# Performance work log

Measured on AMD Instinct MI355X. Metric: run time of the kernel, lower is better.

The kernel has to match this reference:

```python
import jax, jax.numpy as jnp
import numpy as np
from jax import lax

B, T = 256, 256
FD = (768, 74, 35)      # text, audio, vision input feature dims
HD = (128, 64, 64)      # LSTM hidden sizes
LEN = sum(HD)           # 256, fused feature dim
TW = 2                  # time_window
EXT = TW * LEN + 1      # 513, extended_dim
RANK = 24
OUT = 1


def setup_inputs() -> dict:
    key = jax.random.key(0)
    ks = iter(jax.random.split(key, 32))
    def n(shape, scale=0.05):
        return jax.random.normal(next(ks), shape, dtype=jnp.float32) * scale
    inp = {
        "text": n((B, T, FD[0]), 1.0),
        "audio": n((B, T, FD[1]), 1.0),
        "vision": n((B, T, FD[2]), 1.0),
    }
    # LSTM params per subnet: W_ih [4H, D], W_hh [4H, H], combined bias [4H]
    for tag, d, h in (("t", FD[0], HD[0]), ("a", FD[1], HD[1]), ("v", FD[2], HD[2])):
        inp[f"Wih_{tag}"] = n((4 * h, d))
        inp[f"Whh_{tag}"] = n((4 * h, h))
        inp[f"b_{tag}"] = n((4 * h,))
    inp["W1"] = n((RANK * OUT, LEN))
    inp["b1"] = n((RANK * OUT,))
    inp["W2"] = n((RANK * OUT, EXT))
    inp["b2"] = n((RANK * OUT,))
    inp["fw"] = n((1, RANK), 1.0)  # fusion_weights, xavier_normal-like
    return inp


def _lstm_seq(x, Wih, Whh, b):
    # x: [B, T, D] -> all hidden states [B, T, H]; torch gate order i,f,g,o
    Bn = x.shape[0]
    H = Whh.shape[1]
    h0 = jnp.zeros((Bn, H), x.dtype)
    def step(carry, xt):
        h, c = carry
        g = xt @ Wih.T + h @ Whh.T + b
        i, f, gg, o = jnp.split(g, 4, axis=-1)
        c = jax.nn.sigmoid(f) * c + jax.nn.sigmoid(i) * jnp.tanh(gg)
        h = jax.nn.sigmoid(o) * jnp.tanh(c)
        return (h, c), h
    _, hs = lax.scan(step, (h0, h0), jnp.swapaxes(x, 0, 1))
    return jnp.swapaxes(hs, 0, 1)


def reference(text, audio, vision,
              Wih_t, Whh_t, b_t, Wih_a, Whh_a, b_a, Wih_v, Whh_v, b_v,
              W1, b1, W2, b2, fw):
    # SubNets (dropout is identity in eval mode)
    audio_h = _lstm_seq(audio, Wih_a, Whh_a, b_a)
    video_h = _lstm_seq(vision, Wih_v, Whh_v, b_v)
    text_h = _lstm_seq(text, Wih_t, Whh_t, b_t)
    z = jnp.concatenate((audio_h, video_h, text_h), axis=2)  # [B, T, LEN]
    # time_extend with time_window=2: [ones, z[:, i], z[:, (i+1) % T]]
    ones = jnp.ones((z.shape[0], z.shape[1], 1), z.dtype)
    shifts = [jnp.roll(z, -j, axis=1) for j in range(TW)]
    z_ext = jnp.concatenate([ones] + shifts, axis=2)  # [B, T, EXT]
    # fusion loop over idx (stride=1 -> all T), vectorized as batched GEMM + mean
    a = jnp.einsum('btl,rl->btr', z, W1) + b1          # [B, T, RANK*OUT]
    bb = jnp.einsum('bte,re->btr', z_ext, W2) + b2     # [B, T, RANK*OUT]
    z_fusion = (a * bb).mean(axis=1)                   # sum_i/len(idx)
    z_fusion = z_fusion.reshape(-1, RANK, OUT)
    z_output = jnp.einsum('r,bro->bo', fw[0], z_fusion)
    output = z_output.reshape(-1, OUT)
    norm = jnp.sum(jnp.linalg.norm(z.reshape(z.shape[0], -1), axis=1)) / z.shape[0]
    return output, norm
```

## Files before the change

### kernel.cpp

```cpp
#include <hip/hip_runtime.h>
#include <math.h>


typedef unsigned short ushortT;
typedef short bf16x8 __attribute__((ext_vector_type(8)));
typedef float f32x4 __attribute__((ext_vector_type(4)));

__device__ __forceinline__ unsigned int f2bf(float f) {
  unsigned int u = __float_as_uint(f);
  u += 0x7FFFu + ((u >> 16) & 1u);
  return u >> 16;
}
__device__ __forceinline__ unsigned int pk2bf(float lo, float hi) {
  return f2bf(lo) | (f2bf(hi) << 16);
}
__device__ __forceinline__ float bf2f(ushortT u) {
  return __uint_as_float(((unsigned int)u) << 16);
}

template <int KP, int KIN, int HR>
__device__ __forceinline__ void cvt_range(const float* __restrict__ src,
                                          ushortT* __restrict__ dst,
                                          int i, int total) {
  if (i >= total) return;
  if constexpr (HR == 0 && KP == KIN) {
    dst[i] = (ushortT)f2bf(src[i]);
  } else {
    const int row = i / KP, c = i - row * KP;
    const int srow = HR ? ((row & 3) * HR + (row >> 2)) : row;
    const float v = (c < KIN) ? src[(size_t)srow * KIN + c] : 0.f;
    dst[i] = (ushortT)f2bf(v);
  }
}

__global__ __launch_bounds__(256) void prep_k(
    const float* __restrict__ Wih_t, const float* __restrict__ Whh_t,
    const float* __restrict__ Wih_a, const float* __restrict__ Whh_a,
    const float* __restrict__ Wih_v, const float* __restrict__ Whh_v,
    const float* __restrict__ audio, const float* __restrict__ vision,
    const float* __restrict__ W2,
    ushortT* __restrict__ Wt768, ushortT* __restrict__ WhhT16,
    ushortT* __restrict__ WA16, ushortT* __restrict__ WhhA16,
    ushortT* __restrict__ WV16, ushortT* __restrict__ WhhV16,
    ushortT* __restrict__ A16a, ushortT* __restrict__ A16v,
    float* __restrict__ w2a, float* __restrict__ w2b, float* __restrict__ w2c) {
  const int b = blockIdx.x, tid = threadIdx.x;
  if (b < 1536)       cvt_range<768, 768, 128>(Wih_t, Wt768, b * 256 + tid, 393216);
  else if (b < 1792)  cvt_range<128, 128, 0>(Whh_t, WhhT16, (b - 1536) * 256 + tid, 65536);
  else if (b < 1856)  cvt_range<64, 64, 0>(Whh_a, WhhA16, (b - 1792) * 256 + tid, 16384);
  else if (b < 1920)  cvt_range<64, 64, 0>(Whh_v, WhhV16, (b - 1856) * 256 + tid, 16384);
  else if (b < 2016)  cvt_range<96, 74, 64>(Wih_a, WA16, (b - 1920) * 256 + tid, 24576);
  else if (b < 2080)  cvt_range<64, 35, 64>(Wih_v, WV16, (b - 2016) * 256 + tid, 16384);
  else if (b < 26656) cvt_range<96, 74, 0>(audio, A16a, (b - 2080) * 256 + tid, 6291456);
  else if (b < 43040) cvt_range<64, 35, 0>(vision, A16v, (b - 26656) * 256 + tid, 4194304);
  else {
    const int i = (b - 43040) * 256 + tid;
    if (i < 12312) {
      const int dg = i / 513, c = i - dg * 513;
      const float v = W2[i];
      if (c == 0) w2c[dg] = v;
      else if (c <= 256) w2a[dg * 256 + c - 1] = v;
      else w2b[dg * 256 + c - 257] = v;
    }
  }
}

#define SA2 40
__global__ __launch_bounds__(512) void gemm_text2_k(const float* __restrict__ X,
                                                    const ushortT* __restrict__ W16,
                                                    const float* __restrict__ bias,
                                                    ushortT* __restrict__ Y16) {
  const int K = 768, N = 512;
  __shared__ __align__(16) ushortT As[128 * SA2];
  __shared__ __align__(16) ushortT Bs[256 * SA2];
  const unsigned int lin = blockIdx.x;
  const int gb = (int)(lin >> 4), rb = (int)(lin & 15);
  const int m0 = (gb * 8 + (rb & 7)) * 128;
  const int n0 = (rb >> 3) * 256;
  const int tid = threadIdx.x;
  const int wave = tid >> 6, lane = tid & 63;
  const int wr = wave >> 2, wc = wave & 3;
  const int lm = lane & 15, lq = lane >> 4;
  const int arow = tid >> 2, aq = (tid & 3) * 8;
  const int brow = tid >> 1, bq = (tid & 1) * 16;

  const float*   Xp = X + (size_t)(m0 + arow) * K + aq;
  const ushortT* Wp = W16 + (size_t)(n0 + brow) * K + bq;
  uint4* As_w = (uint4*)&As[arow * SA2 + aq];
  uint4* Bs_w = (uint4*)&Bs[brow * SA2 + bq];

  f32x4 acc[4][4];
#pragma unroll
  for (int i = 0; i < 4; i++)
#pragma unroll
    for (int j = 0; j < 4; j++) acc[i][j] = (f32x4){0.f, 0.f, 0.f, 0.f};

  float4 a0 = *(const float4*)(Xp);
  float4 a1 = *(const float4*)(Xp + 4);
  uint4 b0v = *(const uint4*)(Wp);
  uint4 b1v = *(const uint4*)(Wp + 8);

  for (int k0 = 0; k0 < K; k0 += 32) {
    __syncthreads();
    uint4 ao;
    ao.x = pk2bf(a0.x, a0.y); ao.y = pk2bf(a0.z, a0.w);
    ao.z = pk2bf(a1.x, a1.y); ao.w = pk2bf(a1.z, a1.w);
    As_w[0] = ao;
    Bs_w[0] = b0v;
    Bs_w[1] = b1v;
    if (k0 + 32 < K) {
      a0 = *(const float4*)(Xp + k0 + 32);
      a1 = *(const float4*)(Xp + k0 + 36);
      b0v = *(const uint4*)(Wp + k0 + 32);
      b1v = *(const uint4*)(Wp + k0 + 40);
    }
    __syncthreads();
    bf16x8 af[4], bfv[4];
#pragma unroll
    for (int mt = 0; mt < 4; mt++)
      af[mt] = *(const bf16x8*)&As[(wr * 64 + mt * 16 + lm) * SA2 + lq * 8];
#pragma unroll
    for (int nt = 0; nt < 4; nt++)
      bfv[nt] = *(const bf16x8*)&Bs[(wc * 64 + nt * 16 + lm) * SA2 + lq * 8];
#pragma unroll
    for (int mt = 0; mt < 4; mt++)
#pragma unroll
      for (int nt = 0; nt < 4; nt++)
        acc[mt][nt] = __builtin_amdgcn_mfma_f32_16x16x32_bf16(af[mt], bfv[nt], acc[mt][nt], 0, 0, 0);
  }
  float biasv[4];
#pragma unroll
  for (int nt = 0; nt < 4; nt++) {
    const int C = n0 + wc * 64 + nt * 16 + lm;
    biasv[nt] = bias[((C & 3) << 7) + (C >> 2)];
  }
#pragma unroll
  for (int mt = 0; mt < 4; mt++) {
#pragma unroll
    for (int nt = 0; nt < 4; nt++) {
      const int row0 = m0 + wr * 64 + mt * 16 + lq * 4;
      const int col = n0 + wc * 64 + nt * 16 + lm;
#pragma unroll
      for (int r = 0; r < 4; r++)
        Y16[(size_t)(row0 + r) * N + col] = (ushortT)f2bf(acc[mt][nt][r] + biasv[nt]);
    }
  }
}

template <int KP, int LOG2H>
__device__ __forceinline__ void gemm_xp_impl(const ushortT* __restrict__ A16,
                                             const ushortT* __restrict__ B16,
                                             const float* __restrict__ bias,
                                             ushortT* __restrict__ Y16,
                                             ushortT* As, ushortT* Bs) {
  constexpr int SB = KP + 8;
  const int n0 = blockIdx.x * 128;
  const int m0 = blockIdx.y * 128;
  const int tid = threadIdx.x;
  const int srow = tid >> 1, shalf = tid & 1;
  const int wave = tid >> 6, lane = tid & 63;
  const int wr = wave >> 1, wc = wave & 1;
  const int lm = lane & 15, lq = lane >> 4;

  const uint4* ap = (const uint4*)(A16 + (size_t)(m0 + srow) * KP + shalf * (KP / 2));
  const uint4* bp = (const uint4*)(B16 + (size_t)(n0 + srow) * KP + shalf * (KP / 2));
  uint4* aw = (uint4*)&As[srow * SB + shalf * (KP / 2)];
  uint4* bw = (uint4*)&Bs[srow * SB + shalf * (KP / 2)];
#pragma unroll
  for (int i = 0; i < KP / 16; i++) { aw[i] = ap[i]; bw[i] = bp[i]; }
  __syncthreads();

  constexpr int KC = KP / 32;
  f32x4 acc[4][4];
#pragma unroll
  for (int i = 0; i < 4; i++)
#pragma unroll
    for (int j = 0; j < 4; j++) acc[i][j] = (f32x4){0.f, 0.f, 0.f, 0.f};
#pragma unroll
  for (int ks = 0; ks < KC; ks++) {
    bf16x8 af[4], bfv[4];
#pragma unroll
    for (int mt = 0; mt < 4; mt++)
      af[mt] = *(const bf16x8*)&As[(wr * 64 + mt * 16 + lm) * SB + ks * 32 + lq * 8];
#pragma unroll
    for (int nt = 0; nt < 4; nt++)
      bfv[nt] = *(const bf16x8*)&Bs[(wc * 64 + nt * 16 + lm) * SB + ks * 32 + lq * 8];
#pragma unroll
    for (int mt = 0; mt < 4; mt++)
#pragma unroll
      for (int nt = 0; nt < 4; nt++)
        acc[mt][nt] = __builtin_amdgcn_mfma_f32_16x16x32_bf16(af[mt], bfv[nt], acc[mt][nt], 0, 0, 0);
  }
  float biasv[4];
#pragma unroll
  for (int nt = 0; nt < 4; nt++) {
    const int C = n0 + wc * 64 + nt * 16 + lm;
    biasv[nt] = bias[((C & 3) << LOG2H) + (C >> 2)];
  }
#pragma unroll
  for (int mt = 0; mt < 4; mt++) {
#pragma unroll
    for (int nt = 0; nt < 4; nt++) {
      const int row0 = m0 + wr * 64 + mt * 16 + lq * 4;
      const int col = n0 + wc * 64 + nt * 16 + lm;
#pragma unroll
      for (int r = 0; r < 4; r++)
        Y16[(size_t)(row0 + r) * 256 + col] = (ushortT)f2bf(acc[mt][nt][r] + biasv[nt]);
    }
  }
}

__global__ __launch_bounds__(256) void gemm_av_k(const ushortT* __restrict__ A16a,
                                                 const ushortT* __restrict__ WA16,
                                                 const float* __restrict__ b_a,
                                                 ushortT* __restrict__ xpa,
                                                 const ushortT* __restrict__ A16v,
                                                 const ushortT* __restrict__ WV16,
                                                 const float* __restrict__ b_v,
                                                 ushortT* __restrict__ xpv) {
  __shared__ __align__(16) ushortT As[128 * 104];
  __shared__ __align__(16) ushortT Bs[128 * 104];
  if (blockIdx.z == 0) gemm_xp_impl<96, 6>(A16a, WA16, b_a, xpa, As, Bs);
  else gemm_xp_impl<64, 6>(A16v, WV16, b_v, xpv, As, Bs);
}

__device__ __forceinline__ void bar_lgkm() {
  asm volatile("s_waitcnt lgkmcnt(0)" ::: "memory");
  __builtin_amdgcn_sched_barrier(0);
  __builtin_amdgcn_s_barrier();
  __builtin_amdgcn_sched_barrier(0);
}

template <int H, int COFF, int CW>
__device__ __forceinline__ void recur_impl5(const ushortT* __restrict__ xp,
                                            const ushortT* __restrict__ Whh,
                                            ushortT* __restrict__ z,
                                            int bblk, char* smem_) {
  constexpr int KC = H / 32;
  constexpr int C4H = 4 * H;
  constexpr int HP = H + 8;
  constexpr int RING = 6;
  constexpr int CRB = H / 8;
  constexpr int FPT = (64 * CRB) / 512;
  constexpr int RS = 256 * C4H;
  ushortT* hbuf = (ushortT*)smem_;
  const int tid = threadIdx.x;
  const int s = tid >> 6, lane = tid & 63;
  const int lm = lane & 15, lq = lane >> 4;
  const int b0 = bblk * 16;
  const bool comp = (s < CW);
  const ushortT* xb = xp + (size_t)(b0 + lq * 4) * RS + (s * 16 + lm) * 4;

  bf16x8 bw[4][KC];
  if (comp) {
#pragma unroll
    for (int g = 0; g < 4; g++)
#pragma unroll
      for (int kc = 0; kc < KC; kc++) {
        const int n = g * H + s * 16 + lm;
        bw[g][kc] = *(const bf16x8*)(Whh + (size_t)n * H + kc * 32 + lq * 8);
      }
  }
  for (int i = tid; i < 16 * HP; i += 512) hbuf[(RING - 1) * 16 * HP + i] = 0;

  uint2 gA[4], gB[4];
  if (comp) {
#pragma unroll
    for (int r = 0; r < 4; r++) {
      gA[r] = *(const uint2*)(xb + (size_t)r * RS);
      gB[r] = *(const uint2*)(xb + (size_t)r * RS + C4H);
    }
  }
  float cst[4] = {0.f, 0.f, 0.f, 0.f};
  __syncthreads();

  auto step = [&](int t, uint2 (&gCur)[4]) {
    if (t >= 4 && (t & 3) == 0) {
      const int t0 = t - 4;
#pragma unroll
      for (int i = 0; i < FPT; i++) {
        const int q = i * 512 + tid;
        const int m = q / (4 * CRB), j = (q / CRB) & 3, cr = q % CRB;
        const uint4 v = *(const uint4*)&hbuf[((t0 + j) % RING) * 16 * HP + m * HP + cr * 8];
        *(uint4*)&z[((size_t)(b0 + m) * 256 + t0 + j) * 256 + COFF + cr * 8] = v;
      }
    }
    if (comp) {
      float ad[4][4];
#pragma unroll
      for (int r = 0; r < 4; r++) {
        const unsigned int w0 = gCur[r].x, w1 = gCur[r].y;
        ad[0][r] = __uint_as_float(w0 << 16);
        ad[1][r] = __uint_as_float(w0 & 0xffff0000u);
        ad[2][r] = __uint_as_float(w1 << 16);
        ad[3][r] = __uint_as_float(w1 & 0xffff0000u);
      }
      const int tn = (t + 2 < 256) ? t + 2 : 255;
#pragma unroll
      for (int r = 0; r < 4; r++)
        gCur[r] = *(const uint2*)(xb + (size_t)r * RS + (size_t)tn * C4H);
      const ushortT* hb = &hbuf[((t + RING - 1) % RING) * 16 * HP + lm * HP];
      bf16x8 af[KC];
#pragma unroll
      for (int kc = 0; kc < KC; kc++) af[kc] = *(const bf16x8*)(hb + kc * 32 + lq * 8);
      f32x4 acc[4];
#pragma unroll
      for (int g = 0; g < 4; g++) acc[g] = (f32x4){0.f, 0.f, 0.f, 0.f};
#pragma unroll
      for (int kc = 0; kc < KC; kc++)
#pragma unroll
        for (int g = 0; g < 4; g++)
          acc[g] = __builtin_amdgcn_mfma_f32_16x16x32_bf16(af[kc], bw[g][kc], acc[g], 0, 0, 0);
      ushortT* hw = &hbuf[(t % RING) * 16 * HP];
      const int col = s * 16 + lm;
#pragma unroll
      for (int r = 0; r < 4; r++) {
        const float iv = acc[0][r] + ad[0][r];
        const float fv = acc[1][r] + ad[1][r];
        const float gg = acc[2][r] + ad[2][r];
        const float ov = acc[3][r] + ad[3][r];
        const float ei = __expf(-iv), ef = __expf(-fv), eg = __expf(-2.f * gg);
        const float pi = 1.f + ei, pf = 1.f + ef, pg = 1.f + eg;
        const float cc = (cst[r] * pi * pg + (1.f - eg) * pf) *
                         __builtin_amdgcn_rcpf(pf * pi * pg);
        cst[r] = cc;
        const float ec = __expf(-2.f * cc), eo = __expf(-ov);
        const float hv = (1.f - ec) * __builtin_amdgcn_rcpf((1.f + eo) * (1.f + ec));
        hw[(lq * 4 + r) * HP + col] = (ushortT)f2bf(hv);
      }
    }
    bar_lgkm();
  };

  for (int t = 0; t < 256; t += 2) {
    step(t, gA);
    step(t + 1, gB);
  }
  {
    const int t0 = 252;
#pragma unroll
    for (int i = 0; i < FPT; i++) {
      const int q = i * 512 + tid;
      const int m = q / (4 * CRB), j = (q / CRB) & 3, cr = q % CRB;
      const uint4 v = *(const uint4*)&hbuf[((t0 + j) % RING) * 16 * HP + m * HP + cr * 8];
      *(uint4*)&z[((size_t)(b0 + m) * 256 + t0 + j) * 256 + COFF + cr * 8] = v;
    }
  }
}

__global__ __launch_bounds__(512, 1) void recur5_k(const ushortT* __restrict__ xpt,
                                                   const ushortT* __restrict__ xpa,
                                                   const ushortT* __restrict__ xpv_,
                                                   const ushortT* __restrict__ Wt,
                                                   const ushortT* __restrict__ Wa,
                                                   const ushortT* __restrict__ Wv,
                                                   ushortT* __restrict__ z) {
  extern __shared__ char smem[];
  const int bid = blockIdx.x;
  if (bid < 16) recur_impl5<128, 128, 8>(xpt, Wt, z, bid, smem);
  else if (bid < 32) recur_impl5<64, 0, 4>(xpa, Wa, z, bid - 16, smem);
  else recur_impl5<64, 64, 4>(xpv_, Wv, z, bid - 32, smem);
}

__global__ __launch_bounds__(192) void fusion_k(const ushortT* __restrict__ z,
                                                const float* __restrict__ W1,
                                                const float* __restrict__ b1,
                                                const float* __restrict__ w2a,
                                                const float* __restrict__ w2b,
                                                const float* __restrict__ w2c,
                                                const float* __restrict__ b2,
                                                const float* __restrict__ fw,
                                                float* __restrict__ s_acc,
                                                float* __restrict__ sumsq) {
  __shared__ __align__(16) float zs[256 * 36];
  __shared__ float red[8];
  const int tid = threadIdx.x;
  const int b = blockIdx.x >> 3;
  const int t0 = (blockIdx.x & 7) * 32;
  const ushortT* zb = z + (size_t)b * 65536;
  float sq = 0.0f;
  for (int idx = tid; idx < 33 * 256; idx += 192) {
    const int row = idx >> 8, k = idx & 255;
    int t = t0 + row; if (t >= 256) t -= 256;
    const float v = bf2f(zb[t * 256 + k]);
    zs[k * 36 + row] = v;
    if (row < 32) sq += v * v;
  }
  __syncthreads();
  const int dg = tid >> 3;
  const int rg = tid & 7;
  const float* w1p = W1 + dg * 256;
  const float* w2ap = w2a + dg * 256;
  const float* w2bp = w2b + dg * 256;
  float aa[4] = {}, ab1[4] = {}, ab2[4] = {};
  for (int k = 0; k < 256; k += 4) {
    const float4 w1v4  = *(const float4*)(w1p + k);
    const float4 w21v4 = *(const float4*)(w2ap + k);
    const float4 w22v4 = *(const float4*)(w2bp + k);
#define FUS_STEP(J, W1C, W21C, W22C)                                   \
    {                                                                  \
      const float* zr = &zs[(k + J) * 36 + (rg << 2)];                 \
      const float4 za = *(const float4*)zr;                            \
      const float z4 = zr[4];                                          \
      aa[0] += za.x * (W1C); aa[1] += za.y * (W1C);                    \
      aa[2] += za.z * (W1C); aa[3] += za.w * (W1C);                    \
      ab1[0] += za.x * (W21C); ab1[1] += za.y * (W21C);                \
      ab1[2] += za.z * (W21C); ab1[3] += za.w * (W21C);                \
      ab2[0] += za.y * (W22C); ab2[1] += za.z * (W22C);                \
      ab2[2] += za.w * (W22C); ab2[3] += z4 * (W22C);                  \
    }
    FUS_STEP(0, w1v4.x, w21v4.x, w22v4.x)
    FUS_STEP(1, w1v4.y, w21v4.y, w22v4.y)
    FUS_STEP(2, w1v4.z, w21v4.z, w22v4.z)
    FUS_STEP(3, w1v4.w, w21v4.w, w22v4.w)
#undef FUS_STEP
  }
  const float b1v = b1[dg];
  const float b2v = b2[dg] + w2c[dg];
  const float fwv = fw[dg];
  float s = 0.0f;
#pragma unroll
  for (int i = 0; i < 4; i++) {
    const float a  = aa[i] + b1v;
    const float bb = ab1[i] + ab2[i] + b2v;
    s += a * bb;
  }
  s *= fwv;
#pragma unroll
  for (int off = 32; off > 0; off >>= 1) {
    s  += __shfl_down(s, off);
    sq += __shfl_down(sq, off);
  }
  const int wid = tid >> 6;
  if ((tid & 63) == 0) { red[wid * 2] = s; red[wid * 2 + 1] = sq; }
  __syncthreads();
  if (tid == 0) {
    atomicAdd(&s_acc[b], red[0] + red[2] + red[4]);
    atomicAdd(&sumsq[b], red[1] + red[3] + red[5]);
  }
}

__global__ __launch_bounds__(256) void final_k(const float* __restrict__ s_acc,
                                               const float* __restrict__ sumsq,
                                               float* __restrict__ out) {
  __shared__ float red[4];
  const int tid = threadIdx.x;
  out[tid] = s_acc[tid] * (1.0f / 256.0f);
  float sq = sqrtf(sumsq[tid]);
#pragma unroll
  for (int off = 32; off > 0; off >>= 1) sq += __shfl_down(sq, off);
  if ((tid & 63) == 0) red[tid >> 6] = sq;
  __syncthreads();
  if (tid == 0) out[256] = (red[0] + red[1] + red[2] + red[3]) * (1.0f / 256.0f);
}

extern "C" void kernel_launch(void* const* d_in, const int* in_sizes, int n_in,
                              void* d_out, int out_size, void* d_ws, size_t ws_size,
                              hipStream_t stream) {
  const float* text   = (const float*)d_in[0];
  const float* audio  = (const float*)d_in[1];
  const float* vision = (const float*)d_in[2];
  const float* Wih_t  = (const float*)d_in[3];
  const float* Whh_t  = (const float*)d_in[4];
  const float* b_t    = (const float*)d_in[5];
  const float* Wih_a  = (const float*)d_in[6];
  const float* Whh_a  = (const float*)d_in[7];
  const float* b_a    = (const float*)d_in[8];
  const float* Wih_v  = (const float*)d_in[9];
  const float* Whh_v  = (const float*)d_in[10];
  const float* b_v    = (const float*)d_in[11];
  const float* W1     = (const float*)d_in[12];
  const float* b1     = (const float*)d_in[13];
  const float* W2     = (const float*)d_in[14];
  const float* b2     = (const float*)d_in[15];
  const float* fw     = (const float*)d_in[16];

  ushortT* xpt = (ushortT*)d_ws;
  ushortT* xpa = xpt + (size_t)33554432;
  ushortT* xpv = xpa + (size_t)16777216;
  ushortT* z16 = xpv + (size_t)16777216;
  float* s_acc = (float*)(z16 + (size_t)16777216);
  float* sumsq = s_acc + 256;
  ushortT* WhhT16 = (ushortT*)(sumsq + 256);
  ushortT* WhhA16 = WhhT16 + 65536;
  ushortT* WhhV16 = WhhA16 + 16384;
  float* w2a = (float*)(WhhV16 + 16384);
  float* w2b = w2a + 6144;
  float* w2c = w2b + 6144;
  ushortT* A16a  = z16;
  ushortT* A16v  = A16a + (size_t)6291456;
  ushortT* Wt768 = A16v + (size_t)4194304;
  ushortT* WA16  = Wt768 + 393216;
  ushortT* WV16  = WA16 + 24576;

  hipMemsetAsync(s_acc, 0, 512 * sizeof(float), stream);

  prep_k<<<43089, 256, 0, stream>>>(Wih_t, Whh_t, Wih_a, Whh_a, Wih_v, Whh_v,
                                    audio, vision, W2,
                                    Wt768, WhhT16, WA16, WhhA16, WV16, WhhV16,
                                    A16a, A16v, w2a, w2b, w2c);

  gemm_text2_k<<<1024, 512, 0, stream>>>(text, Wt768, b_t, xpt);
  gemm_av_k<<<dim3(2, 512, 2), 256, 0, stream>>>(A16a, WA16, b_a, xpa,
                                                 A16v, WV16, b_v, xpv);
  recur5_k<<<48, 512, 26112, stream>>>(xpt, xpa, xpv, WhhT16, WhhA16, WhhV16, z16);
  fusion_k<<<2048, 192, 0, stream>>>(z16, W1, b1, w2a, w2b, w2c, b2, fw, s_acc, sumsq);
  final_k<<<1, 256, 0, stream>>>(s_acc, sumsq, (float*)d_out);
}
```

Baseline: 750.5 us.

## Fold gate scaling into weights, fuse input conversion, merge final reduction into fusion

Pre-scales the recurrent weights and input projections by -log2(e) (and twice that for the g gate), so the LSTM cell can call v_exp_f32 directly and drops the per-step multiplies. The audio and vision bf16 conversions move from prep_k into the input-projection GEMM, removing a large intermediate write and read. The memset and final_k launches are replaced by zeroing in prep_k and a last-block-done reduction inside fusion_k. fusion_k now loads z as vectorised uint2. The pre-scaling also bf16-rounds the scaled values, which slightly changes numerics.

```diff
diff --git a/kernel.cpp b/kernel.cpp
--- a/kernel.cpp
+++ b/kernel.cpp
@@ -5,6 +5,11 @@
 typedef unsigned short ushortT;
 typedef short bf16x8 __attribute__((ext_vector_type(8)));
 typedef float f32x4 __attribute__((ext_vector_type(4)));
+typedef float f32x2 __attribute__((ext_vector_type(2)));
+typedef float f4u __attribute__((ext_vector_type(4), aligned(4)));
+
+#define K1C (-1.4426950408889634f)
+#define K2C (-2.885390081777927f)
 
 __device__ __forceinline__ unsigned int f2bf(float f) {
   unsigned int u = __float_as_uint(f);
@@ -17,44 +22,55 @@
 __device__ __forceinline__ float bf2f(ushortT u) {
   return __uint_as_float(((unsigned int)u) << 16);
 }
+__device__ __forceinline__ float exp2i(float x) {
+  float r; asm("v_exp_f32 %0, %1" : "=v"(r) : "v"(x)); return r;
+}
+__device__ __forceinline__ unsigned int cvtbf(float x) {
+  unsigned int r;
+  asm("v_cvt_pk_bf16_f32 %0, %1, %2" : "=v"(r) : "v"(x), "v"(x));
+  return r;
+}
 
 template <int KP, int KIN, int HR>
-__device__ __forceinline__ void cvt_range(const float* __restrict__ src,
-                                          ushortT* __restrict__ dst,
-                                          int i, int total) {
+__device__ __forceinline__ void cvt_perm(const float* __restrict__ src,
+                                         ushortT* __restrict__ dst,
+                                         int i, int total) {
   if (i >= total) return;
-  if constexpr (HR == 0 && KP == KIN) {
-    dst[i] = (ushortT)f2bf(src[i]);
-  } else {
-    const int row = i / KP, c = i - row * KP;
-    const int srow = HR ? ((row & 3) * HR + (row >> 2)) : row;
-    const float v = (c < KIN) ? src[(size_t)srow * KIN + c] : 0.f;
-    dst[i] = (ushortT)f2bf(v);
-  }
+  const int row = i / KP, c = i - row * KP;
+  const int srow = HR ? ((row & 3) * HR + (row >> 2)) : row;
+  const float v = (c < KIN) ? src[(size_t)srow * KIN + c] : 0.f;
+  dst[i] = (ushortT)f2bf(v);
+}
+template <int GSH>
+__device__ __forceinline__ void cvt_whh(const float* __restrict__ src,
+                                        ushortT* __restrict__ dst,
+                                        int i, int total) {
+  if (i >= total) return;
+  const int g = (i >> GSH) & 3;
+  const float sc = (g == 2) ? K2C : K1C;
+  dst[i] = (ushortT)f2bf(src[i] * sc);
 }
 
 __global__ __launch_bounds__(256) void prep_k(
     const float* __restrict__ Wih_t, const float* __restrict__ Whh_t,
     const float* __restrict__ Wih_a, const float* __restrict__ Whh_a,
     const float* __restrict__ Wih_v, const float* __restrict__ Whh_v,
-    const float* __restrict__ audio, const float* __restrict__ vision,
     const float* __restrict__ W2,
     ushortT* __restrict__ Wt768, ushortT* __restrict__ WhhT16,
     ushortT* __restrict__ WA16, ushortT* __restrict__ WhhA16,
     ushortT* __restrict__ WV16, ushortT* __restrict__ WhhV16,
-    ushortT* __restrict__ A16a, ushortT* __restrict__ A16v,
-    float* __restrict__ w2a, float* __restrict__ w2b, float* __restrict__ w2c) {
+    float* __restrict__ w2a, float* __restrict__ w2b, float* __restrict__ w2c,
+    float* __restrict__ s_acc, float* __restrict__ sumsq,
+    unsigned int* __restrict__ cnt) {
   const int b = blockIdx.x, tid = threadIdx.x;
-  if (b < 1536)       cvt_range<768, 768, 128>(Wih_t, Wt768, b * 256 + tid, 393216);
-  else if (b < 1792)  cvt_range<128, 128, 0>(Whh_t, WhhT16, (b - 1536) * 256 + tid, 65536);
-  else if (b < 1856)  cvt_range<64, 64, 0>(Whh_a, WhhA16, (b - 1792) * 256 + tid, 16384);
-  else if (b < 1920)  cvt_range<64, 64, 0>(Whh_v, WhhV16, (b - 1856) * 256 + tid, 16384);
-  else if (b < 2016)  cvt_range<96, 74, 64>(Wih_a, WA16, (b - 1920) * 256 + tid, 24576);
-  else if (b < 2080)  cvt_range<64, 35, 64>(Wih_v, WV16, (b - 2016) * 256 + tid, 16384);
-  else if (b < 26656) cvt_range<96, 74, 0>(audio, A16a, (b - 2080) * 256 + tid, 6291456);
-  else if (b < 43040) cvt_range<64, 35, 0>(vision, A16v, (b - 26656) * 256 + tid, 4194304);
-  else {
-    const int i = (b - 43040) * 256 + tid;
+  if (b < 1536)       cvt_perm<768, 768, 128>(Wih_t, Wt768, b * 256 + tid, 393216);
+  else if (b < 1792)  cvt_whh<14>(Whh_t, WhhT16, (b - 1536) * 256 + tid, 65536);
+  else if (b < 1856)  cvt_whh<12>(Whh_a, WhhA16, (b - 1792) * 256 + tid, 16384);
+  else if (b < 1920)  cvt_whh<12>(Whh_v, WhhV16, (b - 1856) * 256 + tid, 16384);
+  else if (b < 2016)  cvt_perm<96, 74, 64>(Wih_a, WA16, (b - 1920) * 256 + tid, 24576);
+  else if (b < 2080)  cvt_perm<64, 35, 64>(Wih_v, WV16, (b - 2016) * 256 + tid, 16384);
+  else if (b < 2129) {
+    const int i = (b - 2080) * 256 + tid;
     if (i < 12312) {
       const int dg = i / 513, c = i - dg * 513;
       const float v = W2[i];
@@ -62,6 +78,10 @@
       else if (c <= 256) w2a[dg * 256 + c - 1] = v;
       else w2b[dg * 256 + c - 257] = v;
     }
+  } else {
+    s_acc[tid] = 0.f;
+    sumsq[tid] = 0.f;
+    if (tid == 0) *cnt = 0u;
   }
 }
 
@@ -128,11 +148,13 @@
       for (int nt = 0; nt < 4; nt++)
         acc[mt][nt] = __builtin_amdgcn_mfma_f32_16x16x32_bf16(af[mt], bfv[nt], acc[mt][nt], 0, 0, 0);
   }
-  float biasv[4];
+  float biasv[4], scv[4];
 #pragma unroll
   for (int nt = 0; nt < 4; nt++) {
     const int C = n0 + wc * 64 + nt * 16 + lm;
-    biasv[nt] = bias[((C & 3) << 7) + (C >> 2)];
+    const int g = C & 3;
+    biasv[nt] = bias[(g << 7) + (C >> 2)];
+    scv[nt] = (g == 2) ? K2C : K1C;
   }
 #pragma unroll
   for (int mt = 0; mt < 4; mt++) {
@@ -142,32 +164,45 @@
       const int col = n0 + wc * 64 + nt * 16 + lm;
 #pragma unroll
       for (int r = 0; r < 4; r++)
-        Y16[(size_t)(row0 + r) * N + col] = (ushortT)f2bf(acc[mt][nt][r] + biasv[nt]);
-    }
-  }
-}
-
-template <int KP, int LOG2H>
-__device__ __forceinline__ void gemm_xp_impl(const ushortT* __restrict__ A16,
-                                             const ushortT* __restrict__ B16,
-                                             const float* __restrict__ bias,
-                                             ushortT* __restrict__ Y16,
-                                             ushortT* As, ushortT* Bs) {
+        Y16[(size_t)(row0 + r) * N + col] = (ushortT)f2bf((acc[mt][nt][r] + biasv[nt]) * scv[nt]);
+    }
+  }
+}
+
+template <int KP, int KIN, int LOG2H>
+__device__ __forceinline__ void gemm_xpf_impl(const float* __restrict__ X,
+                                              const ushortT* __restrict__ B16,
+                                              const float* __restrict__ bias,
+                                              ushortT* __restrict__ Y16,
+                                              ushortT* As, ushortT* Bs) {
   constexpr int SB = KP + 8;
   const int n0 = blockIdx.x * 128;
   const int m0 = blockIdx.y * 128;
   const int tid = threadIdx.x;
-  const int srow = tid >> 1, shalf = tid & 1;
   const int wave = tid >> 6, lane = tid & 63;
   const int wr = wave >> 1, wc = wave & 1;
   const int lm = lane & 15, lq = lane >> 4;
 
-  const uint4* ap = (const uint4*)(A16 + (size_t)(m0 + srow) * KP + shalf * (KP / 2));
-  const uint4* bp = (const uint4*)(B16 + (size_t)(n0 + srow) * KP + shalf * (KP / 2));
-  uint4* aw = (uint4*)&As[srow * SB + shalf * (KP / 2)];
-  uint4* bw = (uint4*)&Bs[srow * SB + shalf * (KP / 2)];
-#pragma unroll
-  for (int i = 0; i < KP / 16; i++) { aw[i] = ap[i]; bw[i] = bp[i]; }
+  for (int idx = tid; idx < 128 * (KP / 4); idx += 256) {
+    const int row = idx / (KP / 4), c0 = (idx % (KP / 4)) * 4;
+    f4u v = {0.f, 0.f, 0.f, 0.f};
+    const int rem = KIN - c0;
+    const float* xr = X + (size_t)(m0 + row) * KIN + c0;
+    if (rem >= 4) v = *(const f4u*)xr;
+    else if (rem > 0) {
+      v.x = xr[0];
+      if (rem > 1) v.y = xr[1];
+      if (rem > 2) v.z = xr[2];
+    }
+    uint2 pk;
+    pk.x = pk2bf(v.x, v.y);
+    pk.y = pk2bf(v.z, v.w);
+    *(uint2*)&As[row * SB + c0] = pk;
+  }
+  for (int idx = tid; idx < 128 * (KP / 8); idx += 256) {
+    const int row = idx / (KP / 8), sg = idx % (KP / 8);
+    *(uint4*)&Bs[row * SB + sg * 8] = *(const uint4*)(B16 + (size_t)row * KP + sg * 8);
+  }
   __syncthreads();
 
   constexpr int KC = KP / 32;
@@ -191,11 +226,13 @@
       for (int nt = 0; nt < 4; nt++)
         acc[mt][nt] = __builtin_amdgcn_mfma_f32_16x16x32_bf16(af[mt], bfv[nt], acc[mt][nt], 0, 0, 0);
   }
-  float biasv[4];
+  float biasv[4], scv[4];
 #pragma unroll
   for (int nt = 0; nt < 4; nt++) {
     const int C = n0 + wc * 64 + nt * 16 + lm;
-    biasv[nt] = bias[((C & 3) << LOG2H) + (C >> 2)];
+    const int g = C & 3;
+    biasv[nt] = bias[(g << LOG2H) + (C >> 2)];
+    scv[nt] = (g == 2) ? K2C : K1C;
   }
 #pragma unroll
   for (int mt = 0; mt < 4; mt++) {
@@ -205,23 +242,23 @@
       const int col = n0 + wc * 64 + nt * 16 + lm;
 #pragma unroll
       for (int r = 0; r < 4; r++)
-        Y16[(size_t)(row0 + r) * 256 + col] = (ushortT)f2bf(acc[mt][nt][r] + biasv[nt]);
-    }
-  }
-}
-
-__global__ __launch_bounds__(256) void gemm_av_k(const ushortT* __restrict__ A16a,
-                                                 const ushortT* __restrict__ WA16,
-                                                 const float* __restrict__ b_a,
-                                                 ushortT* __restrict__ xpa,
-                                                 const ushortT* __restrict__ A16v,
-                                                 const ushortT* __restrict__ WV16,
-                                                 const float* __restrict__ b_v,
-                                                 ushortT* __restrict__ xpv) {
+        Y16[(size_t)(row0 + r) * 256 + col] = (ushortT)f2bf((acc[mt][nt][r] + biasv[nt]) * scv[nt]);
+    }
+  }
+}
+
+__global__ __launch_bounds__(256) void gemm_avf_k(const float* __restrict__ audio,
+                                                  const ushortT* __restrict__ WA16,
+                                                  const float* __restrict__ b_a,
+                                                  ushortT* __restrict__ xpa,
+                                                  const float* __restrict__ vision,
+                                                  const ushortT* __restrict__ WV16,
+                                                  const float* __restrict__ b_v,
+                                                  ushortT* __restrict__ xpv) {
   __shared__ __align__(16) ushortT As[128 * 104];
   __shared__ __align__(16) ushortT Bs[128 * 104];
-  if (blockIdx.z == 0) gemm_xp_impl<96, 6>(A16a, WA16, b_a, xpa, As, Bs);
-  else gemm_xp_impl<64, 6>(A16v, WV16, b_v, xpv, As, Bs);
+  if (blockIdx.z == 0) gemm_xpf_impl<96, 74, 6>(audio, WA16, b_a, xpa, As, Bs);
+  else gemm_xpf_impl<64, 35, 6>(vision, WV16, b_v, xpv, As, Bs);
 }
 
 __device__ __forceinline__ void bar_lgkm() {
@@ -232,7 +269,7 @@
 }
 
 template <int H, int COFF, int CW>
-__device__ __forceinline__ void recur_impl5(const ushortT* __restrict__ xp,
+__device__ __forceinline__ void recur_impl6(const ushortT* __restrict__ xp,
                                             const ushortT* __restrict__ Whh,
                                             ushortT* __restrict__ z,
                                             int bblk, char* smem_) {
@@ -286,14 +323,14 @@
       }
     }
     if (comp) {
-      float ad[4][4];
+      f32x4 ad0, ad1, ad2, ad3;
 #pragma unroll
       for (int r = 0; r < 4; r++) {
         const unsigned int w0 = gCur[r].x, w1 = gCur[r].y;
-        ad[0][r] = __uint_as_float(w0 << 16);
-        ad[1][r] = __uint_as_float(w0 & 0xffff0000u);
-        ad[2][r] = __uint_as_float(w1 << 16);
-        ad[3][r] = __uint_as_float(w1 & 0xffff0000u);
+        ad0[r] = __uint_as_float(w0 << 16);
+        ad1[r] = __uint_as_float(w0 & 0xffff0000u);
+        ad2[r] = __uint_as_float(w1 << 16);
+        ad3[r] = __uint_as_float(w1 & 0xffff0000u);
       }
       const int tn = (t + 2 < 256) ? t + 2 : 255;
 #pragma unroll
@@ -314,19 +351,31 @@
       ushortT* hw = &hbuf[(t % RING) * 16 * HP];
       const int col = s * 16 + lm;
 #pragma unroll
-      for (int r = 0; r < 4; r++) {
-        const float iv = acc[0][r] + ad[0][r];
-        const float fv = acc[1][r] + ad[1][r];
-        const float gg = acc[2][r] + ad[2][r];
-        const float ov = acc[3][r] + ad[3][r];
-        const float ei = __expf(-iv), ef = __expf(-fv), eg = __expf(-2.f * gg);
-        const float pi = 1.f + ei, pf = 1.f + ef, pg = 1.f + eg;
-        const float cc = (cst[r] * pi * pg + (1.f - eg) * pf) *
-                         __builtin_amdgcn_rcpf(pf * pi * pg);
-        cst[r] = cc;
-        const float ec = __expf(-2.f * cc), eo = __expf(-ov);
-        const float hv = (1.f - ec) * __builtin_amdgcn_rcpf((1.f + eo) * (1.f + ec));
-        hw[(lq * 4 + r) * HP + col] = (ushortT)f2bf(hv);
+      for (int p = 0; p < 2; p++) {
+        const int r0 = 2 * p, r1 = 2 * p + 1;
+        f32x2 iv = { acc[0][r0] + ad0[r0], acc[0][r1] + ad0[r1] };
+        f32x2 fv = { acc[1][r0] + ad1[r0], acc[1][r1] + ad1[r1] };
+        f32x2 gv = { acc[2][r0] + ad2[r0], acc[2][r1] + ad2[r1] };
+        f32x2 ov = { acc[3][r0] + ad3[r0], acc[3][r1] + ad3[r1] };
+        f32x2 ei = { exp2i(iv.x), exp2i(iv.y) };
+        f32x2 ef = { exp2i(fv.x), exp2i(fv.y) };
+        f32x2 eg = { exp2i(gv.x), exp2i(gv.y) };
+        f32x2 pi = ei + 1.f, pf = ef + 1.f, pg = eg + 1.f;
+        f32x2 t1 = pi * pg;
+        f32x2 cst2 = { cst[r0], cst[r1] };
+        f32x2 num = cst2 * t1 + (1.f - eg) * pf;
+        f32x2 den = pf * t1;
+        f32x2 cc = { num.x * __builtin_amdgcn_rcpf(den.x),
+                     num.y * __builtin_amdgcn_rcpf(den.y) };
+        cst[r0] = cc.x; cst[r1] = cc.y;
+        f32x2 eo = { exp2i(ov.x), exp2i(ov.y) };
+        f32x2 ec = { exp2i(cc.x * K2C), exp2i(cc.y * K2C) };
+        f32x2 hn = 1.f - ec;
+        f32x2 hd = (eo + 1.f) * (ec + 1.f);
+        const float h0 = hn.x * __builtin_amdgcn_rcpf(hd.x);
+        const float h1 = hn.y * __builtin_amdgcn_rcpf(hd.y);
+        hw[(lq * 4 + r0) * HP + col] = (ushortT)cvtbf(h0);
+        hw[(lq * 4 + r1) * HP + col] = (ushortT)cvtbf(h1);
       }
     }
     bar_lgkm();
@@ -348,7 +397,7 @@
   }
 }
 
-__global__ __launch_bounds__(512, 1) void recur5_k(const ushortT* __restrict__ xpt,
+__global__ __launch_bounds__(512, 1) void recur6_k(const ushortT* __restrict__ xpt,
                                                    const ushortT* __restrict__ xpa,
                                                    const ushortT* __restrict__ xpv_,
                                                    const ushortT* __restrict__ Wt,
@@ -357,9 +406,9 @@
                                                    ushortT* __restrict__ z) {
   extern __shared__ char smem[];
   const int bid = blockIdx.x;
-  if (bid < 16) recur_impl5<128, 128, 8>(xpt, Wt, z, bid, smem);
-  else if (bid < 32) recur_impl5<64, 0, 4>(xpa, Wa, z, bid - 16, smem);
-  else recur_impl5<64, 64, 4>(xpv_, Wv, z, bid - 32, smem);
+  if (bid < 16) recur_impl6<128, 128, 8>(xpt, Wt, z, bid, smem);
+  else if (bid < 32) recur_impl6<64, 0, 4>(xpa, Wa, z, bid - 16, smem);
+  else recur_impl6<64, 64, 4>(xpv_, Wv, z, bid - 32, smem);
 }
 
 __global__ __launch_bounds__(192) void fusion_k(const ushortT* __restrict__ z,
@@ -371,20 +420,28 @@
                                                 const float* __restrict__ b2,
                                                 const float* __restrict__ fw,
                                                 float* __restrict__ s_acc,
-                                                float* __restrict__ sumsq) {
+                                                float* __restrict__ sumsq,
+                                                unsigned int* __restrict__ cnt,
+                                                float* __restrict__ out) {
   __shared__ __align__(16) float zs[256 * 36];
-  __shared__ float red[8];
+  __shared__ float red[12];
+  __shared__ unsigned int done_s;
   const int tid = threadIdx.x;
   const int b = blockIdx.x >> 3;
   const int t0 = (blockIdx.x & 7) * 32;
   const ushortT* zb = z + (size_t)b * 65536;
   float sq = 0.0f;
-  for (int idx = tid; idx < 33 * 256; idx += 192) {
-    const int row = idx >> 8, k = idx & 255;
+  for (int idx = tid; idx < 33 * 64; idx += 192) {
+    const int row = idx >> 6, kq = idx & 63;
     int t = t0 + row; if (t >= 256) t -= 256;
-    const float v = bf2f(zb[t * 256 + k]);
-    zs[k * 36 + row] = v;
-    if (row < 32) sq += v * v;
+    const uint2 v = *(const uint2*)(zb + t * 256 + kq * 4);
+    const float f0 = __uint_as_float(v.x << 16);
+    const float f1 = __uint_as_float(v.x & 0xffff0000u);
+    const float f2 = __uint_as_float(v.y << 16);
+    const float f3 = __uint_as_float(v.y & 0xffff0000u);
+    const int base = kq * 4 * 36 + row;
+    zs[base] = f0; zs[base + 36] = f1; zs[base + 72] = f2; zs[base + 108] = f3;
+    if (row < 32) sq += f0 * f0 + f1 * f1 + f2 * f2 + f3 * f3;
   }
   __syncthreads();
   const int dg = tid >> 3;
@@ -437,21 +494,25 @@
   if (tid == 0) {
     atomicAdd(&s_acc[b], red[0] + red[2] + red[4]);
     atomicAdd(&sumsq[b], red[1] + red[3] + red[5]);
-  }
-}
-
-__global__ __launch_bounds__(256) void final_k(const float* __restrict__ s_acc,
-                                               const float* __restrict__ sumsq,
-                                               float* __restrict__ out) {
-  __shared__ float red[4];
-  const int tid = threadIdx.x;
-  out[tid] = s_acc[tid] * (1.0f / 256.0f);
-  float sq = sqrtf(sumsq[tid]);
-#pragma unroll
-  for (int off = 32; off > 0; off >>= 1) sq += __shfl_down(sq, off);
-  if ((tid & 63) == 0) red[tid >> 6] = sq;
+    __threadfence();
+    done_s = atomicAdd(cnt, 1u);
+  }
   __syncthreads();
-  if (tid == 0) out[256] = (red[0] + red[1] + red[2] + red[3]) * (1.0f / 256.0f);
+  if (done_s == 2047) {
+    __threadfence();
+    float sl = 0.f;
+    for (int i = tid; i < 256; i += 192) {
+      const float sa = __hip_atomic_load(&s_acc[i], __ATOMIC_RELAXED, __HIP_MEMORY_SCOPE_AGENT);
+      const float sb = __hip_atomic_load(&sumsq[i], __ATOMIC_RELAXED, __HIP_MEMORY_SCOPE_AGENT);
+      out[i] = sa * (1.0f / 256.0f);
+      sl += sqrtf(sb);
+    }
+#pragma unroll
+    for (int off = 32; off > 0; off >>= 1) sl += __shfl_down(sl, off);
+    if ((tid & 63) == 0) red[6 + (tid >> 6)] = sl;
+    __syncthreads();
+    if (tid == 0) out[256] = (red[6] + red[7] + red[8]) * (1.0f / 256.0f);
+  }
 }
 
 extern "C" void kernel_launch(void* const* d_in, const int* in_sizes, int n_in,
@@ -487,23 +548,19 @@
   float* w2a = (float*)(WhhV16 + 16384);
   float* w2b = w2a + 6144;
   float* w2c = w2b + 6144;
-  ushortT* A16a  = z16;
-  ushortT* A16v  = A16a + (size_t)6291456;
-  ushortT* Wt768 = A16v + (size_t)4194304;
+  unsigned int* cnt = (unsigned int*)(w2c + 24);
+  ushortT* Wt768 = z16;
   ushortT* WA16  = Wt768 + 393216;
   ushortT* WV16  = WA16 + 24576;
 
-  hipMemsetAsync(s_acc, 0, 512 * sizeof(float), stream);
-
-  prep_k<<<43089, 256, 0, stream>>>(Wih_t, Whh_t, Wih_a, Whh_a, Wih_v, Whh_v,
-                                    audio, vision, W2,
-                                    Wt768, WhhT16, WA16, WhhA16, WV16, WhhV16,
-                                    A16a, A16v, w2a, w2b, w2c);
+  prep_k<<<2130, 256, 0, stream>>>(Wih_t, Whh_t, Wih_a, Whh_a, Wih_v, Whh_v, W2,
+                                   Wt768, WhhT16, WA16, WhhA16, WV16, WhhV16,
+                                   w2a, w2b, w2c, s_acc, sumsq, cnt);
 
   gemm_text2_k<<<1024, 512, 0, stream>>>(text, Wt768, b_t, xpt);
-  gemm_av_k<<<dim3(2, 512, 2), 256, 0, stream>>>(A16a, WA16, b_a, xpa,
-                                                 A16v, WV16, b_v, xpv);
-  recur5_k<<<48, 512, 26112, stream>>>(xpt, xpa, xpv, WhhT16, WhhA16, WhhV16, z16);
-  fusion_k<<<2048, 192, 0, stream>>>(z16, W1, b1, w2a, w2b, w2c, b2, fw, s_acc, sumsq);
-  final_k<<<1, 256, 0, stream>>>(s_acc, sumsq, (float*)d_out);
-}
+  gemm_avf_k<<<dim3(2, 512, 2), 256, 0, stream>>>(audio, WA16, b_a, xpa,
+                                                  vision, WV16, b_v, xpv);
+  recur6_k<<<48, 512, 26112, stream>>>(xpt, xpa, xpv, WhhT16, WhhA16, WhhV16, z16);
+  fusion_k<<<2048, 192, 0, stream>>>(z16, W1, b1, w2a, w2b, w2c, b2, fw,
+                                     s_acc, sumsq, cnt, (float*)d_out);
+}
```

Result: slower. 800.6 us (+6.7%).
